# Optimization experiments

Measured on AMD Instinct MI355X. Metric: run time of the kernel, lower is better.

Reference implementation:

```python
import jax, jax.numpy as jnp
import numpy as np

DIM = 256
STATE = 64
D_INNER = 256  # ssd_expand=1 * dim
HIDDEN = 1024  # mlp_ratio=4 * dim
EPS = 1e-5


def ln2d(x, w, b):
    # channel LayerNorm over dim 1 of [B,C,H,W]
    u = x.mean(1, keepdims=True)
    s = ((x - u) ** 2).mean(1, keepdims=True)
    return w[None, :, None, None] * ((x - u) * jax.lax.rsqrt(s + EPS)) + b[None, :, None, None]


def dwconv3x3(x, w, b=None):
    # depthwise 3x3, pad 1; x [B,C,H,W], w [C,1,3,3]
    y = jax.lax.conv_general_dilated(
        x, w, (1, 1), [(1, 1), (1, 1)],
        dimension_numbers=("NCHW", "OIHW", "NCHW"),
        feature_group_count=x.shape[1])
    if b is not None:
        y = y + b[None, :, None, None]
    return y


def setup_inputs() -> dict:
    key = jax.random.key(0)
    ks = jax.random.split(key, 20)
    rn = lambda k, shp, s=0.05: (s * jax.random.normal(k, shp)).astype(jnp.float32)
    inp = {
        "x": jax.random.normal(ks[0], (16, DIM, 64, 64), dtype=jnp.float32),
        "alpha": rn(ks[1], (4, DIM), 0.1),
        "ln_w": jnp.ones((DIM,)), "ln_b": jnp.zeros((DIM,)),
        "dw1_w": rn(ks[2], (DIM, 1, 3, 3), 0.1),
        "dw1_ln_w": jnp.ones((DIM,)), "dw1_ln_b": jnp.zeros((DIM,)),
        "dw2_w": rn(ks[3], (DIM, 1, 3, 3), 0.1),
        "dw2_ln_w": jnp.ones((DIM,)), "dw2_ln_b": jnp.zeros((DIM,)),
        "bcdt_w": rn(ks[4], (3 * STATE, DIM)),
        "bcdt_b": jnp.zeros((3 * STATE,)),
        "dwm_w": rn(ks[5], (3 * STATE, 1, 3, 3), 0.1),
        "dwm_b": jnp.zeros((3 * STATE,)),
        "hz_w": rn(ks[6], (2 * D_INNER, DIM)),
        "hz_b": jnp.zeros((2 * D_INNER,)),
        "outp_w": rn(ks[7], (DIM, D_INNER)),
        "outp_b": jnp.zeros((DIM,)),
        "A": jax.random.uniform(ks[8], (STATE,), minval=1.0, maxval=16.0).astype(jnp.float32),
        "Dp": jnp.ones((DIM,)),
        "fc1_w": rn(ks[9], (HIDDEN, DIM)),
        "fc1_ln_w": jnp.ones((HIDDEN,)), "fc1_ln_b": jnp.zeros((HIDDEN,)),
        "fc2_w": rn(ks[10], (DIM, HIDDEN)),
        "fc2_ln_w": jnp.ones((DIM,)), "fc2_ln_b": jnp.zeros((DIM,)),
    }
    return inp


def reference(x, alpha, ln_w, ln_b, dw1_w, dw1_ln_w, dw1_ln_b, dw2_w, dw2_ln_w, dw2_ln_b,
              bcdt_w, bcdt_b, dwm_w, dwm_b, hz_w, hz_b, outp_w, outp_b, A, Dp,
              fc1_w, fc1_ln_w, fc1_ln_b, fc2_w, fc2_ln_w, fc2_ln_b):
    a = jax.nn.sigmoid(alpha)[:, None, :, None, None]  # [4,1,dim,1,1]

    # sub-layer 1: depthwise conv + LN, gated residual
    x1 = (1.0 - a[0]) * x + a[0] * ln2d(dwconv3x3(x, dw1_w), dw1_ln_w, dw1_ln_b)

    # HSMSSD mixer on LayerNorm2D(x1)
    xn = ln2d(x1, ln_w, ln_b)
    Bb, Dd, H, W = xn.shape
    L = H * W
    xf = xn.reshape(Bb, Dd, L)
    bcdt = jnp.einsum("oc,bcl->bol", bcdt_w, xf) + bcdt_b[None, :, None]
    bcdt = dwconv3x3(bcdt.reshape(Bb, 3 * STATE, H, W), dwm_w, dwm_b).reshape(Bb, 3 * STATE, L)
    Bm, Cm, dt = jnp.split(bcdt, [STATE, 2 * STATE], axis=1)  # each [B,S,L]
    Asm = jax.nn.softmax(dt + A[None, :, None], axis=-1)
    AB = Asm * Bm
    h = jnp.einsum("bdl,bsl->bds", xf, AB)  # [B,D,S]
    hz = jnp.einsum("oc,bcs->bos", hz_w, h) + hz_b[None, :, None]
    hp, z = jnp.split(hz, [D_INNER], axis=1)
    hg = hp * jax.nn.silu(z)
    ho = jnp.einsum("oc,bcs->bos", outp_w, hg) + outp_b[None, :, None]
    y = jnp.einsum("bds,bsl->bdl", ho, Cm).reshape(Bb, Dd, H, W)
    y = y + xn * Dp[None, :, None, None]

    x2 = (1.0 - a[1]) * x1 + a[1] * y
    x3 = (1.0 - a[2]) * x2 + a[2] * ln2d(dwconv3x3(x2, dw2_w), dw2_ln_w, dw2_ln_b)

    # FFN: 1x1 conv -> LN -> SiLU -> 1x1 conv -> LN
    f1 = jax.nn.silu(ln2d(jnp.einsum("oc,bchw->bohw", fc1_w, x3), fc1_ln_w, fc1_ln_b))
    f2 = ln2d(jnp.einsum("oc,bchw->bohw", fc2_w, f1), fc2_ln_w, fc2_ln_b)
    x4 = (1.0 - a[3]) * x3 + a[3] * f2
    return (x4, h)
```

## Files before the change

### kernel.cpp

```cpp
#include <hip/hip_runtime.h>
#include <math.h>

#define LPOS 4096
#define NB 16

typedef __bf16 bf16;
typedef __bf16 bf16x8 __attribute__((ext_vector_type(8)));
typedef __bf16 bf16x4 __attribute__((ext_vector_type(4)));
typedef float f32x4 __attribute__((ext_vector_type(4)));

#define GLOAD_LDS16(g, l) \
    __builtin_amdgcn_global_load_lds((const __attribute__((address_space(1))) unsigned int*)(g), \
                                     (__attribute__((address_space(3))) unsigned int*)(l), 16, 0, 0)

#define SWZ512(byte) ((byte) ^ (((((unsigned)(byte)) >> 9) & 7) << 4))

__device__ __forceinline__ float sigm(float x){ return 1.f/(1.f+expf(-x)); }

__global__ void dwconv3x3_k(const float* __restrict__ in, const float* __restrict__ w9,
                            const float* __restrict__ bias, float* __restrict__ out, int C)
{
    int bc = blockIdx.x;
    int c = bc % C;
    __shared__ float tile[66][72];
    const float* p = in + (size_t)bc * LPOS;
    int tid = threadIdx.x;
    for (int i = tid; i < 144; i += 256) {
        int r = (i < 72) ? 0 : 65;
        int cc = i % 72;
        tile[r][cc] = 0.f;
    }
    if (tid < 64) { tile[tid+1][3] = 0.f; tile[tid+1][68] = 0.f; }
#pragma unroll
    for (int j = 0; j < 4; j++) {
        int f = tid + j*256;
        int y = f >> 4, x4 = (f & 15) << 2;
        *(f32x4*)&tile[1+y][4+x4] = *(const f32x4*)&p[y*64 + x4];
    }
    __syncthreads();
    float w[9];
#pragma unroll
    for (int i = 0; i < 9; i++) w[i] = w9[c*9 + i];
    float bb = bias ? bias[c] : 0.f;
    float* q = out + (size_t)bc * LPOS;
#pragma unroll
    for (int j = 0; j < 4; j++) {
        int f = tid + j*256;
        int y = f >> 4, x4 = (f & 15) << 2;
        f32x4 acc = {bb, bb, bb, bb};
#pragma unroll
        for (int dy = 0; dy < 3; dy++) {
            const float* row = &tile[y+dy][3 + x4];
            float t0 = row[0], t1 = row[1], t2 = row[2];
            float t3 = row[3], t4 = row[4], t5 = row[5];
            float w0 = w[dy*3], w1 = w[dy*3+1], w2 = w[dy*3+2];
            acc[0] += w0*t0 + w1*t1 + w2*t2;
            acc[1] += w0*t1 + w1*t2 + w2*t3;
            acc[2] += w0*t2 + w1*t3 + w2*t4;
            acc[3] += w0*t3 + w1*t4 + w2*t5;
        }
        *(f32x4*)&q[y*64 + x4] = acc;
    }
}

__global__ __launch_bounds__(512)
void ln_x1xn_k(const float* __restrict__ conv, const float* __restrict__ xin,
               float* __restrict__ x1, bf16* __restrict__ xnC, bf16* __restrict__ xnT,
               const float* __restrict__ dww, const float* __restrict__ dwb,
               const float* __restrict__ g0,
               const float* __restrict__ lnw, const float* __restrict__ lnb)
{
    int b = blockIdx.x >> 6;
    int tx = threadIdx.x;
    int ty = threadIdx.y;
    int p0 = ((blockIdx.x & 63) << 6) + (tx << 2);
    __shared__ float rs[32][68], rs2[32][68];
    int tid = ty*16 + tx;
    f32x4 vals[8];
    f32x4 s = {0.f,0.f,0.f,0.f}, s2 = {0.f,0.f,0.f,0.f};
    size_t bi = ((size_t)b*256 + ty*8)*LPOS + p0;
#pragma unroll
    for (int i = 0; i < 8; i++) {
        f32x4 x = *(const f32x4*)&conv[bi + (size_t)i*LPOS];
        vals[i] = x; s += x; s2 += x*x;
    }
#pragma unroll
    for (int q = 0; q < 4; q++) { rs[ty][tx*4+q] = s[q]; rs2[ty][tx*4+q] = s2[q]; }
    __syncthreads();
    {
        int r = tid >> 6, cc = tid & 63;
        rs[r][cc]  = rs[r][cc]  + rs[r+8][cc]  + rs[r+16][cc]  + rs[r+24][cc];
        rs2[r][cc] = rs2[r][cc] + rs2[r+8][cc] + rs2[r+16][cc] + rs2[r+24][cc];
    }
    __syncthreads();
    f32x4 S = {0.f,0.f,0.f,0.f}, S2 = {0.f,0.f,0.f,0.f};
#pragma unroll
    for (int j = 0; j < 8; j++) {
        S  += *(const f32x4*)&rs[j][tx*4];
        S2 += *(const f32x4*)&rs2[j][tx*4];
    }
    f32x4 u, inv;
#pragma unroll
    for (int q = 0; q < 4; q++) {
        float uu = S[q]*(1.f/256.f);
        u[q] = uu;
        inv[q] = rsqrtf(S2[q]*(1.f/256.f) - uu*uu + 1e-5f);
    }
    __syncthreads();
    s = (f32x4){0.f,0.f,0.f,0.f}; s2 = (f32x4){0.f,0.f,0.f,0.f};
#pragma unroll
    for (int i = 0; i < 8; i++) {
        int c = ty*8 + i;
        float w = dww[c], bbc = dwb[c];
        float g = sigm(g0[c]);
        f32x4 xv = *(const f32x4*)&xin[bi + (size_t)i*LPOS];
        f32x4 r;
#pragma unroll
        for (int q = 0; q < 4; q++) {
            float ln = w*((vals[i][q]-u[q])*inv[q]) + bbc;
            r[q] = (1.f-g)*xv[q] + g*ln;
        }
        vals[i] = r;
        *(f32x4*)&x1[bi + (size_t)i*LPOS] = r;
        s += r; s2 += r*r;
    }
#pragma unroll
    for (int q = 0; q < 4; q++) { rs[ty][tx*4+q] = s[q]; rs2[ty][tx*4+q] = s2[q]; }
    __syncthreads();
    {
        int r = tid >> 6, cc = tid & 63;
        rs[r][cc]  = rs[r][cc]  + rs[r+8][cc]  + rs[r+16][cc]  + rs[r+24][cc];
        rs2[r][cc] = rs2[r][cc] + rs2[r+8][cc] + rs2[r+16][cc] + rs2[r+24][cc];
    }
    __syncthreads();
    S = (f32x4){0.f,0.f,0.f,0.f}; S2 = (f32x4){0.f,0.f,0.f,0.f};
#pragma unroll
    for (int j = 0; j < 8; j++) {
        S  += *(const f32x4*)&rs[j][tx*4];
        S2 += *(const f32x4*)&rs2[j][tx*4];
    }
#pragma unroll
    for (int q = 0; q < 4; q++) {
        float uu = S[q]*(1.f/256.f);
        u[q] = uu;
        inv[q] = rsqrtf(S2[q]*(1.f/256.f) - uu*uu + 1e-5f);
    }
    bf16 tmp[32];
#pragma unroll
    for (int i = 0; i < 8; i++) {
        int c = ty*8 + i;
        float w = lnw[c], bbc = lnb[c];
        bf16x4 o;
#pragma unroll
        for (int q = 0; q < 4; q++) {
            float xnv = w*((vals[i][q]-u[q])*inv[q]) + bbc;
            o[q] = (bf16)xnv;
            tmp[q*8+i] = (bf16)xnv;
        }
        *(bf16x4*)&xnC[bi + (size_t)i*LPOS] = o;
    }
#pragma unroll
    for (int q = 0; q < 4; q++) {
        bf16x8* dst = (bf16x8*)&xnT[((size_t)b*LPOS + p0 + q)*256 + ty*8];
        *dst = *(bf16x8*)&tmp[q*8];
    }
}

__global__ __launch_bounds__(512)
void ln2d_k(const float* __restrict__ v, const float* __restrict__ base,
            float* __restrict__ out, const float* __restrict__ lnw,
            const float* __restrict__ lnb, const float* __restrict__ gate,
            bf16* __restrict__ auxT, int mode)
{
    int b = blockIdx.x >> 6;
    int tx = threadIdx.x;
    int ty = threadIdx.y;
    int p0 = ((blockIdx.x & 63) << 6) + (tx << 2);
    __shared__ float rs[32][68], rs2[32][68];
    int tid = ty*16 + tx;
    f32x4 vals[8];
    f32x4 s = {0.f,0.f,0.f,0.f}, s2 = {0.f,0.f,0.f,0.f};
    size_t bi = ((size_t)b*256 + ty*8)*LPOS + p0;
#pragma unroll
    for (int i = 0; i < 8; i++) {
        f32x4 x = *(const f32x4*)&v[bi + (size_t)i*LPOS];
        vals[i] = x; s += x; s2 += x*x;
    }
#pragma unroll
    for (int q = 0; q < 4; q++) { rs[ty][tx*4+q] = s[q]; rs2[ty][tx*4+q] = s2[q]; }
    __syncthreads();
    {
        int r = tid >> 6, cc = tid & 63;
        rs[r][cc]  = rs[r][cc]  + rs[r+8][cc]  + rs[r+16][cc]  + rs[r+24][cc];
        rs2[r][cc] = rs2[r][cc] + rs2[r+8][cc] + rs2[r+16][cc] + rs2[r+24][cc];
    }
    __syncthreads();
    f32x4 S = {0.f,0.f,0.f,0.f}, S2 = {0.f,0.f,0.f,0.f};
#pragma unroll
    for (int j = 0; j < 8; j++) {
        S  += *(const f32x4*)&rs[j][tx*4];
        S2 += *(const f32x4*)&rs2[j][tx*4];
    }
    f32x4 u, inv;
#pragma unroll
    for (int q = 0; q < 4; q++) {
        float uu = S[q]*(1.f/256.f);
        u[q] = uu;
        inv[q] = rsqrtf(S2[q]*(1.f/256.f) - uu*uu + 1e-5f);
    }
    bf16 tmp[32];
#pragma unroll
    for (int i = 0; i < 8; i++) {
        int c = ty*8 + i;
        float w = lnw[c], bbc = lnb[c];
        f32x4 r;
        if (mode == 0) {
#pragma unroll
            for (int q = 0; q < 4; q++) r[q] = w*((vals[i][q]-u[q])*inv[q]) + bbc;
        } else {
            float g = sigm(gate[c]);
            f32x4 bs = *(const f32x4*)&base[bi + (size_t)i*LPOS];
#pragma unroll
            for (int q = 0; q < 4; q++) {
                float ln = w*((vals[i][q]-u[q])*inv[q]) + bbc;
                r[q] = (1.f-g)*bs[q] + g*ln;
            }
        }
        *(f32x4*)&out[bi + (size_t)i*LPOS] = r;
#pragma unroll
        for (int q = 0; q < 4; q++) tmp[q*8+i] = (bf16)r[q];
    }
    if (auxT) {
#pragma unroll
        for (int q = 0; q < 4; q++) {
            bf16x8* dst = (bf16x8*)&auxT[((size_t)b*LPOS + p0 + q)*256 + ty*8];
            *dst = *(bf16x8*)&tmp[q*8];
        }
    }
}

__global__ void f2b_k(const float* __restrict__ in, bf16* __restrict__ out, int n)
{
    int i = blockIdx.x*256 + threadIdx.x;
    if (i < n) out[i] = (bf16)in[i];
}

__global__ void pad_w_k(const float* __restrict__ w, bf16* __restrict__ out)
{
    int i = blockIdx.x*256 + threadIdx.x;
    int r = i >> 8;
    out[i] = (r < 192) ? (bf16)w[(size_t)r*256 + (i & 255)] : (bf16)0.f;
}

__global__ void transpose_cm_k(const float* __restrict__ Cm, bf16* __restrict__ CmT)
{
    int b = blockIdx.y;
    int l0 = blockIdx.x * 64;
    const float* src = Cm + (size_t)b * 192 * LPOS;
    bf16* dst = CmT + (size_t)b * LPOS * 64;
    __shared__ float t[64][65];
    int tid = threadIdx.x;
    for (int i = tid; i < 4096; i += 256) {
        int s = i >> 6, l = i & 63;
        t[s][l] = src[(size_t)s*LPOS + l0 + l];
    }
    __syncthreads();
    for (int i = tid; i < 4096; i += 256) {
        int l = i >> 6, s = i & 63;
        dst[(size_t)(l0+l)*64 + s] = (bf16)t[s][l];
    }
}

__global__ void softmax_ab_k(const float* __restrict__ bcdt2, bf16* __restrict__ ABb,
                             const float* __restrict__ Avec)
{
    int b = blockIdx.x >> 6, s = blockIdx.x & 63;
    size_t base = (size_t)b*192*LPOS;
    const f32x4* dt = (const f32x4*)(bcdt2 + base + (size_t)(128+s)*LPOS);
    const f32x4* Bm = (const f32x4*)(bcdt2 + base + (size_t)s*LPOS);
    bf16* outp = ABb + ((size_t)b*64 + s)*LPOS;
    int tid = threadIdx.x;
    float av = Avec[s];
    f32x4 v[4];
    float mx = -1e30f;
#pragma unroll
    for (int i = 0; i < 4; i++) {
        f32x4 x = dt[tid + (i<<8)];
#pragma unroll
        for (int q = 0; q < 4; q++) { x[q] += av; mx = fmaxf(mx, x[q]); }
        v[i] = x;
    }
    __shared__ float red[256];
    red[tid] = mx; __syncthreads();
    for (int o = 128; o > 0; o >>= 1) {
        if (tid < o) red[tid] = fmaxf(red[tid], red[tid+o]);
        __syncthreads();
    }
    mx = red[0];
    __syncthreads();
    float sum = 0.f;
#pragma unroll
    for (int i = 0; i < 4; i++)
#pragma unroll
        for (int q = 0; q < 4; q++) { v[i][q] = expf(v[i][q]-mx); sum += v[i][q]; }
    red[tid] = sum; __syncthreads();
    for (int o = 128; o > 0; o >>= 1) {
        if (tid < o) red[tid] += red[tid+o];
        __syncthreads();
    }
    float rinv = 1.f / red[0];
#pragma unroll
    for (int i = 0; i < 4; i++) {
        f32x4 bm = Bm[tid + (i<<8)];
        bf16x4 o;
#pragma unroll
        for (int q = 0; q < 4; q++) o[q] = (bf16)(v[i][q] * rinv * bm[q]);
        ((bf16x4*)outp)[tid + (i<<8)] = o;
    }
}

__global__ __launch_bounds__(512)
void mixer_tail_k(const float* __restrict__ h, const float* __restrict__ hz_w,
                  const float* __restrict__ hz_b, const float* __restrict__ outp_w,
                  const float* __restrict__ outp_b, bf16* __restrict__ hob16)
{
    __shared__ bf16 hT[64*256];
    __shared__ bf16 hzs[512*64];
    int b = blockIdx.x;
    int tid = threadIdx.x;
    int lane = tid & 63, w = tid >> 6;
    int fm = lane & 15, quad = lane >> 4;

    const float* hb = h + (size_t)b*256*64;
#pragma unroll
    for (int j = 0; j < 8; j++) {
        int e4 = tid + j*512;
        f32x4 v = *(const f32x4*)&hb[e4*4];
        int k = (e4*4) >> 6;
        int n = (e4*4) & 63;
#pragma unroll
        for (int q = 0; q < 4; q++) {
            int byte = (n+q)*512 + k*2;
            *(bf16*)((char*)hT + SWZ512(byte)) = (bf16)v[q];
        }
    }
    __syncthreads();

    int mw = w*64;
    f32x4 acc[4][4] = {};
#pragma unroll
    for (int ks = 0; ks < 8; ks++) {
        int k0 = ks*32;
        bf16x8 af[4], bfr[4];
#pragma unroll
        for (int i = 0; i < 4; i++) {
            const float* wp = &hz_w[(size_t)(mw + i*16 + fm)*256 + k0 + quad*8];
            f32x4 w0 = *(const f32x4*)wp;
            f32x4 w1 = *(const f32x4*)(wp + 4);
#pragma unroll
            for (int q = 0; q < 4; q++) { af[i][q] = (bf16)w0[q]; af[i][4+q] = (bf16)w1[q]; }
        }
#pragma unroll
        for (int j = 0; j < 4; j++) {
            int n = j*16 + fm;
            int byte = n*512 + (k0 + quad*8)*2;
            bfr[j] = *(const bf16x8*)((const char*)hT + SWZ512(byte));
        }
#pragma unroll
        for (int i = 0; i < 4; i++)
#pragma unroll
            for (int j = 0; j < 4; j++)
                acc[i][j] = __builtin_amdgcn_mfma_f32_16x16x32_bf16(af[i], bfr[j], acc[i][j], 0, 0, 0);
    }
#pragma unroll
    for (int i = 0; i < 4; i++)
#pragma unroll
        for (int r = 0; r < 4; r++) {
            int m = mw + i*16 + quad*4 + r;
            float bb = hz_b[m];
#pragma unroll
            for (int j = 0; j < 4; j++)
                hzs[m*64 + j*16 + fm] = (bf16)(acc[i][j][r] + bb);
        }
    __syncthreads();

    {
        int k = tid >> 1, n0 = (tid & 1) * 32;
#pragma unroll
        for (int c = 0; c < 4; c++) {
            bf16x8 hp = *(const bf16x8*)&hzs[k*64 + n0 + c*8];
            bf16x8 zz = *(const bf16x8*)&hzs[(k+256)*64 + n0 + c*8];
#pragma unroll
            for (int q = 0; q < 8; q++) {
                float z = (float)zz[q];
                float g = (float)hp[q] * z * sigm(z);
                int byte = (n0 + c*8 + q)*512 + k*2;
                *(bf16*)((char*)hT + SWZ512(byte)) = (bf16)g;
            }
        }
    }
    __syncthreads();

    int mw2 = w*32;
    f32x4 acc2[2][4] = {};
#pragma unroll
    for (int ks = 0; ks < 8; ks++) {
        int k0 = ks*32;
        bf16x8 af[2], bfr[4];
#pragma unroll
        for (int i = 0; i < 2; i++) {
            const float* wp = &outp_w[(size_t)(mw2 + i*16 + fm)*256 + k0 + quad*8];
            f32x4 w0 = *(const f32x4*)wp;
            f32x4 w1 = *(const f32x4*)(wp + 4);
#pragma unroll
            for (int q = 0; q < 4; q++) { af[i][q] = (bf16)w0[q]; af[i][4+q] = (bf16)w1[q]; }
        }
#pragma unroll
        for (int j = 0; j < 4; j++) {
            int n = j*16 + fm;
            int byte = n*512 + (k0 + quad*8)*2;
            bfr[j] = *(const bf16x8*)((const char*)hT + SWZ512(byte));
        }
#pragma unroll
        for (int i = 0; i < 2; i++)
#pragma unroll
            for (int j = 0; j < 4; j++)
                acc2[i][j] = __builtin_amdgcn_mfma_f32_16x16x32_bf16(af[i], bfr[j], acc2[i][j], 0, 0, 0);
    }
    bf16* ob = hob16 + (size_t)b*256*64;
#pragma unroll
    for (int i = 0; i < 2; i++)
#pragma unroll
        for (int r = 0; r < 4; r++) {
            int m = mw2 + i*16 + quad*4 + r;
            float bb = outp_b[m];
#pragma unroll
            for (int j = 0; j < 4; j++)
                ob[m*64 + j*16 + fm] = (bf16)(acc2[i][j][r] + bb);
        }
}

template<int OUT_BF16>
__global__ __launch_bounds__(256)
void gemm_nt_mfma(const bf16* __restrict__ A, const bf16* __restrict__ B,
                  void* __restrict__ C, const float* __restrict__ bias, int mlimit,
                  int K, int lda, int ldb, int ldc,
                  size_t abst, size_t bbst, size_t cbst)
{
    int b = blockIdx.z;
    const bf16* Ab = A + (size_t)b*abst;
    const bf16* Bb = B + (size_t)b*bbst;
    int m0 = blockIdx.y*128, n0 = blockIdx.x*128;
    __shared__ bf16 Asl[128*64];
    __shared__ bf16 Bsl[128*64];
    int tid = threadIdx.x;
    int lane = tid & 63;
    int w = tid >> 6;
    int wm = (w >> 1)*64, wn = (w & 1)*64;
    int fm = lane & 15, quad = lane >> 4;
    f32x4 acc[4][4] = {};
    for (int k0 = 0; k0 < K; k0 += 64) {
#pragma unroll
        for (int ii = 0; ii < 4; ii++) {
            int q = ii*256 + tid;
            int row = q >> 3, ko = (q & 7) << 3;
            GLOAD_LDS16(Ab + (size_t)(m0+row)*lda + k0 + ko, &Asl[q*8]);
            GLOAD_LDS16(Bb + (size_t)(n0+row)*ldb + k0 + ko, &Bsl[q*8]);
        }
        __syncthreads();
#pragma unroll
        for (int kk = 0; kk < 2; kk++) {
            bf16x8 af[4], bfr[4];
#pragma unroll
            for (int i = 0; i < 4; i++)
                af[i] = *(const bf16x8*)&Asl[(wm + i*16 + fm)*64 + kk*32 + quad*8];
#pragma unroll
            for (int j = 0; j < 4; j++)
                bfr[j] = *(const bf16x8*)&Bsl[(wn + j*16 + fm)*64 + kk*32 + quad*8];
#pragma unroll
            for (int i = 0; i < 4; i++)
#pragma unroll
                for (int j = 0; j < 4; j++)
                    acc[i][j] = __builtin_amdgcn_mfma_f32_16x16x32_bf16(af[i], bfr[j], acc[i][j], 0, 0, 0);
        }
        __syncthreads();
    }
    size_t cb = (size_t)b*cbst;
#pragma unroll
    for (int i = 0; i < 4; i++) {
#pragma unroll
        for (int r = 0; r < 4; r++) {
            int m = m0 + wm + i*16 + quad*4 + r;
            if (m >= mlimit) continue;
            float bb = bias ? bias[m] : 0.f;
#pragma unroll
            for (int j = 0; j < 4; j++) {
                int n = n0 + wn + j*16 + fm;
                float vv = acc[i][j][r] + bb;
                if (OUT_BF16) ((bf16*)C)[cb + (size_t)m*ldc + n] = (bf16)vv;
                else          ((float*)C)[cb + (size_t)m*ldc + n] = vv;
            }
        }
    }
}

__global__ __launch_bounds__(256)
void gemm_fc1_stats(const bf16* __restrict__ A, const bf16* __restrict__ B,
                    bf16* __restrict__ C, float* __restrict__ stats)
{
    int z = blockIdx.z;
    const bf16* Ab = A + (size_t)z*LPOS*256;
    bf16* Cb = C + (size_t)z*LPOS*1024;
    int m0 = blockIdx.y*128, n0 = blockIdx.x*128;
    __shared__ bf16 Asl[128*64];
    __shared__ bf16 Bsl[128*64];
    int tid = threadIdx.x;
    int lane = tid & 63;
    int w = tid >> 6;
    int wm = (w >> 1)*64, wn = (w & 1)*64;
    int fm = lane & 15, quad = lane >> 4;
    f32x4 acc[4][4] = {};
    for (int k0 = 0; k0 < 256; k0 += 64) {
#pragma unroll
        for (int ii = 0; ii < 4; ii++) {
            int q = ii*256 + tid;
            int row = q >> 3, ko = (q & 7) << 3;
            GLOAD_LDS16(Ab + (size_t)(m0+row)*256 + k0 + ko, &Asl[q*8]);
            GLOAD_LDS16(B + (size_t)(n0+row)*256 + k0 + ko, &Bsl[q*8]);
        }
        __syncthreads();
#pragma unroll
        for (int kk = 0; kk < 2; kk++) {
            bf16x8 af[4], bfr[4];
#pragma unroll
            for (int i = 0; i < 4; i++)
                af[i] = *(const bf16x8*)&Asl[(wm + i*16 + fm)*64 + kk*32 + quad*8];
#pragma unroll
            for (int j = 0; j < 4; j++)
                bfr[j] = *(const bf16x8*)&Bsl[(wn + j*16 + fm)*64 + kk*32 + quad*8];
#pragma unroll
            for (int i = 0; i < 4; i++)
#pragma unroll
                for (int j = 0; j < 4; j++)
                    acc[i][j] = __builtin_amdgcn_mfma_f32_16x16x32_bf16(af[i], bfr[j], acc[i][j], 0, 0, 0);
        }
        __syncthreads();
    }
#pragma unroll
    for (int i = 0; i < 4; i++) {
#pragma unroll
        for (int r = 0; r < 4; r++) {
            int m = m0 + wm + i*16 + quad*4 + r;
            float s = 0.f, s2 = 0.f;
#pragma unroll
            for (int j = 0; j < 4; j++) {
                int n = n0 + wn + j*16 + fm;
                float vv = acc[i][j][r];
                Cb[(size_t)m*1024 + n] = (bf16)vv;
                s += vv; s2 += vv*vv;
            }
#pragma unroll
            for (int msk = 1; msk <= 8; msk <<= 1) {
                s  += __shfl_xor(s, msk);
                s2 += __shfl_xor(s2, msk);
            }
            if (fm == 0) {
                atomicAdd(&stats[(size_t)(z*LPOS + m)*2 + 0], s);
                atomicAdd(&stats[(size_t)(z*LPOS + m)*2 + 1], s2);
            }
        }
    }
}

__global__ __launch_bounds__(512)
void gemm_fc2_out(const bf16* __restrict__ A, const bf16* __restrict__ f1,
                  const float* __restrict__ stats,
                  const float* __restrict__ l1w, const float* __restrict__ l1b,
                  const float* __restrict__ x3, float* __restrict__ outp,
                  const float* __restrict__ lw, const float* __restrict__ lb,
                  const float* __restrict__ gate)
{
    int z = blockIdx.z;
    const bf16* Bb = f1 + (size_t)z*LPOS*1024;
    const float* x3b = x3 + (size_t)z*256*LPOS;
    float* ob = outp + (size_t)z*256*LPOS;
    int n0 = blockIdx.x*64;
    __shared__ bf16 Asl[256*64];
    __shared__ bf16 Bsl[64*64];
    __shared__ float ps[4][64], ps2[4][64];
    __shared__ float wsl[1024], bsl[1024];
    int tid = threadIdx.x;
    int lane = tid & 63;
    int w = tid >> 6;
    int wm = (w & 3)*64, wn = (w >> 2)*32;
    int fm = lane & 15, quad = lane >> 4;
    for (int i = tid; i < 1024; i += 512) { wsl[i] = l1w[i]; bsl[i] = l1b[i]; }
    int brow = tid >> 3;
    int bko = (tid & 7) << 3;
    float sS = stats[(size_t)(z*LPOS + n0 + brow)*2 + 0];
    float sQ = stats[(size_t)(z*LPOS + n0 + brow)*2 + 1];
    float bu = sS*(1.f/1024.f);
    float binv = rsqrtf(sQ*(1.f/1024.f) - bu*bu + 1e-5f);
    f32x4 acc[4][2] = {};
    for (int k0 = 0; k0 < 1024; k0 += 64) {
#pragma unroll
        for (int ii = 0; ii < 4; ii++) {
            int q = ii*512 + tid;
            int row = q >> 3, ko = (q & 7) << 3;
            GLOAD_LDS16(A + (size_t)row*1024 + k0 + ko, &Asl[q*8]);
        }
        GLOAD_LDS16(Bb + (size_t)(n0+brow)*1024 + k0 + bko, &Bsl[tid*8]);
        __syncthreads();
        {
            bf16x8 v = *(const bf16x8*)&Bsl[tid*8];
            bf16x8 o;
#pragma unroll
            for (int e = 0; e < 8; e++) {
                int k = k0 + bko + e;
                float xx = ((float)v[e] - bu)*binv;
                xx = wsl[k]*xx + bsl[k];
                o[e] = (bf16)(xx*sigm(xx));
            }
            *(bf16x8*)&Bsl[tid*8] = o;
        }
        __syncthreads();
#pragma unroll
        for (int kk = 0; kk < 2; kk++) {
            bf16x8 af[4], bfr[2];
#pragma unroll
            for (int i = 0; i < 4; i++)
                af[i] = *(const bf16x8*)&Asl[(wm + i*16 + fm)*64 + kk*32 + quad*8];
#pragma unroll
            for (int j = 0; j < 2; j++)
                bfr[j] = *(const bf16x8*)&Bsl[(wn + j*16 + fm)*64 + kk*32 + quad*8];
#pragma unroll
            for (int i = 0; i < 4; i++)
#pragma unroll
                for (int j = 0; j < 2; j++)
                    acc[i][j] = __builtin_amdgcn_mfma_f32_16x16x32_bf16(af[i], bfr[j], acc[i][j], 0, 0, 0);
        }
        __syncthreads();
    }
#pragma unroll
    for (int j = 0; j < 2; j++) {
        float s = 0.f, s2 = 0.f;
#pragma unroll
        for (int i = 0; i < 4; i++)
#pragma unroll
            for (int r = 0; r < 4; r++) { float v = acc[i][j][r]; s += v; s2 += v*v; }
        s  += __shfl_xor(s, 16);  s2 += __shfl_xor(s2, 16);
        s  += __shfl_xor(s, 32);  s2 += __shfl_xor(s2, 32);
        if (quad == 0) {
            int n = wn + j*16 + fm;
            ps[w & 3][n] = s;
            ps2[w & 3][n] = s2;
        }
    }
    __syncthreads();
    float us[2], iv[2];
#pragma unroll
    for (int j = 0; j < 2; j++) {
        int n = wn + j*16 + fm;
        float S  = ps[0][n] + ps[1][n] + ps[2][n] + ps[3][n];
        float S2 = ps2[0][n] + ps2[1][n] + ps2[2][n] + ps2[3][n];
        float u = S*(1.f/256.f);
        us[j] = u;
        iv[j] = rsqrtf(S2*(1.f/256.f) - u*u + 1e-5f);
    }
#pragma unroll
    for (int i = 0; i < 4; i++) {
#pragma unroll
        for (int r = 0; r < 4; r++) {
            int m = wm + i*16 + quad*4 + r;
            float g = sigm(gate[m]);
            float lwm = lw[m], lbm = lb[m];
#pragma unroll
            for (int j = 0; j < 2; j++) {
                int n = n0 + wn + j*16 + fm;
                size_t idx = (size_t)m*LPOS + n;
                float ln = lwm*((acc[i][j][r]-us[j])*iv[j]) + lbm;
                ob[idx] = (1.f-g)*x3b[idx] + g*ln;
            }
        }
    }
}

__global__ __launch_bounds__(256)
void gemm_h_mfma(const bf16* __restrict__ xnC, const bf16* __restrict__ ABb,
                 float* __restrict__ h, int Kchunk)
{
    int b = blockIdx.z;
    const bf16* Ab = xnC + (size_t)b*256*LPOS;
    const bf16* Bb = ABb + (size_t)b*64*LPOS;
    float* Cb = h + (size_t)b*256*64;
    int m0 = blockIdx.y*128;
    int kbase = blockIdx.x*Kchunk;
    __shared__ bf16 Asl[128*64];
    __shared__ bf16 Bsl[64*64];
    int tid = threadIdx.x;
    int lane = tid & 63;
    int w = tid >> 6;
    int wm = (w >> 1)*64, wn = (w & 1)*32;
    int fm = lane & 15, quad = lane >> 4;
    f32x4 acc[4][2] = {};
    for (int k0 = kbase; k0 < kbase + Kchunk; k0 += 64) {
#pragma unroll
        for (int ii = 0; ii < 4; ii++) {
            int q = ii*256 + tid;
            int row = q >> 3, ko = (q & 7) << 3;
            GLOAD_LDS16(Ab + (size_t)(m0+row)*LPOS + k0 + ko, &Asl[q*8]);
        }
#pragma unroll
        for (int ii = 0; ii < 2; ii++) {
            int q = ii*256 + tid;
            int row = q >> 3, ko = (q & 7) << 3;
            GLOAD_LDS16(Bb + (size_t)row*LPOS + k0 + ko, &Bsl[q*8]);
        }
        __syncthreads();
#pragma unroll
        for (int kk = 0; kk < 2; kk++) {
            bf16x8 af[4], bfr[2];
#pragma unroll
            for (int i = 0; i < 4; i++)
                af[i] = *(const bf16x8*)&Asl[(wm + i*16 + fm)*64 + kk*32 + quad*8];
#pragma unroll
            for (int j = 0; j < 2; j++)
                bfr[j] = *(const bf16x8*)&Bsl[(wn + j*16 + fm)*64 + kk*32 + quad*8];
#pragma unroll
            for (int i = 0; i < 4; i++)
#pragma unroll
                for (int j = 0; j < 2; j++)
                    acc[i][j] = __builtin_amdgcn_mfma_f32_16x16x32_bf16(af[i], bfr[j], acc[i][j], 0, 0, 0);
        }
        __syncthreads();
    }
#pragma unroll
    for (int i = 0; i < 4; i++)
#pragma unroll
        for (int r = 0; r < 4; r++) {
            int m = m0 + wm + i*16 + quad*4 + r;
#pragma unroll
            for (int j = 0; j < 2; j++) {
                int n = wn + j*16 + fm;
                atomicAdd(&Cb[(size_t)m*64 + n], acc[i][j][r]);
            }
        }
}

__global__ __launch_bounds__(256)
void mixer_out_mfma(const bf16* __restrict__ hoB, const bf16* __restrict__ CmT,
                    const bf16* __restrict__ xnC, float* __restrict__ x,
                    const float* __restrict__ Dp, const float* __restrict__ gate)
{
    int b = blockIdx.z;
    const bf16* Ab = hoB + (size_t)b*(256*64);
    const bf16* Bb = CmT + (size_t)b*((size_t)LPOS*64);
    int m0 = blockIdx.y*128, n0 = blockIdx.x*128;
    __shared__ bf16 Asl[128*64];
    __shared__ bf16 Bsl[128*64];
    int tid = threadIdx.x;
    int lane = tid & 63;
    int w = tid >> 6;
    int wm = (w >> 1)*64, wn = (w & 1)*64;
    int fm = lane & 15, quad = lane >> 4;
    f32x4 acc[4][4] = {};
#pragma unroll
    for (int ii = 0; ii < 4; ii++) {
        int q = ii*256 + tid;
        int row = q >> 3, ko = (q & 7) << 3;
        GLOAD_LDS16(Ab + (size_t)(m0+row)*64 + ko, &Asl[q*8]);
        GLOAD_LDS16(Bb + (size_t)(n0+row)*64 + ko, &Bsl[q*8]);
    }
    __syncthreads();
#pragma unroll
    for (int kk = 0; kk < 2; kk++) {
        bf16x8 af[4], bfr[4];
#pragma unroll
        for (int i = 0; i < 4; i++)
            af[i] = *(const bf16x8*)&Asl[(wm + i*16 + fm)*64 + kk*32 + quad*8];
#pragma unroll
        for (int j = 0; j < 4; j++)
            bfr[j] = *(const bf16x8*)&Bsl[(wn + j*16 + fm)*64 + kk*32 + quad*8];
#pragma unroll
        for (int i = 0; i < 4; i++)
#pragma unroll
            for (int j = 0; j < 4; j++)
                acc[i][j] = __builtin_amdgcn_mfma_f32_16x16x32_bf16(af[i], bfr[j], acc[i][j], 0, 0, 0);
    }
#pragma unroll
    for (int i = 0; i < 4; i++) {
#pragma unroll
        for (int r = 0; r < 4; r++) {
            int m = m0 + wm + i*16 + quad*4 + r;
            float g = sigm(gate[m]);
            float dp = Dp[m];
#pragma unroll
            for (int j = 0; j < 4; j++) {
                int n = n0 + wn + j*16 + fm;
                size_t idx = ((size_t)b*256 + m)*LPOS + n;
                float y = acc[i][j][r] + (float)xnC[idx]*dp;
                x[idx] = (1.f-g)*x[idx] + g*y;
            }
        }
    }
}

extern "C" void kernel_launch(void* const* d_in, const int* in_sizes, int n_in,
                              void* d_out, int out_size, void* d_ws, size_t ws_size,
                              hipStream_t stream)
{
    const float* x        = (const float*)d_in[0];
    const float* alpha    = (const float*)d_in[1];
    const float* ln_w     = (const float*)d_in[2];
    const float* ln_b     = (const float*)d_in[3];
    const float* dw1_w    = (const float*)d_in[4];
    const float* dw1_ln_w = (const float*)d_in[5];
    const float* dw1_ln_b = (const float*)d_in[6];
    const float* dw2_w    = (const float*)d_in[7];
    const float* dw2_ln_w = (const float*)d_in[8];
    const float* dw2_ln_b = (const float*)d_in[9];
    const float* bcdt_w   = (const float*)d_in[10];
    const float* bcdt_b   = (const float*)d_in[11];
    const float* dwm_w    = (const float*)d_in[12];
    const float* dwm_b    = (const float*)d_in[13];
    const float* hz_w     = (const float*)d_in[14];
    const float* hz_b     = (const float*)d_in[15];
    const float* outp_w   = (const float*)d_in[16];
    const float* outp_b   = (const float*)d_in[17];
    const float* Avec     = (const float*)d_in[18];
    const float* Dp       = (const float*)d_in[19];
    const float* fc1_w    = (const float*)d_in[20];
    const float* fc1_ln_w = (const float*)d_in[21];
    const float* fc1_ln_b = (const float*)d_in[22];
    const float* fc2_w    = (const float*)d_in[23];
    const float* fc2_ln_w = (const float*)d_in[24];
    const float* fc2_ln_b = (const float*)d_in[25];

    float* outp  = (float*)d_out;
    float* h_out = outp + (size_t)NB*256*LPOS;

    float* ws   = (float*)d_ws;
    float* bufA = ws;
    float* bufB = bufA + (size_t)NB*256*LPOS;
    float* bufC = bufB + (size_t)NB*256*LPOS;
    float* bufD = bufC + (size_t)NB*256*LPOS;
    float* hzb  = bufD + (size_t)NB*192*LPOS;

    bf16* CmT     = (bf16*)bufA;
    bf16* ABb     = (bf16*)(bufA + 8*1024*1024);
    bf16* xnC     = (bf16*)bufC;
    bf16* xnT     = xnC + (size_t)NB*256*LPOS;
    bf16* f1buf   = (bf16*)bufC;
    bf16* x3t     = (bf16*)bufD;
    bf16* fc1_wb  = (bf16*)(bufD + 9000000);
    bf16* fc2_wb  = (bf16*)(bufD + 9200000);
    bf16* hob16   = (bf16*)(bufD + 9400000);
    float* stats  = bufD + 10000000;
    bf16* wpad    = (bf16*)hzb;

    dim3 blk256(256);
    dim3 blkLN(16, 32);

    dwconv3x3_k<<<dim3(NB*256), blk256, 0, stream>>>(x, dw1_w, nullptr, bufA, 256);
    ln_x1xn_k<<<dim3(NB*64), blkLN, 0, stream>>>(bufA, x, bufB, xnC, xnT,
                                                 dw1_ln_w, dw1_ln_b, alpha + 0, ln_w, ln_b);
    pad_w_k<<<dim3(256), blk256, 0, stream>>>(bcdt_w, wpad);
    gemm_nt_mfma<0><<<dim3(32, 2, NB), blk256, 0, stream>>>(
        wpad, xnT, (void*)bufA, bcdt_b, 192, 256, 256, 256, LPOS,
        0, (size_t)LPOS*256, (size_t)192*LPOS);
    dwconv3x3_k<<<dim3(NB*192), blk256, 0, stream>>>(bufA, dwm_w, dwm_b, bufD, 192);
    transpose_cm_k<<<dim3(64, NB), blk256, 0, stream>>>(bufD + (size_t)64*LPOS, CmT);
    softmax_ab_k<<<dim3(NB*64), blk256, 0, stream>>>(bufD, ABb, Avec);
    hipMemsetAsync(h_out, 0, (size_t)NB*256*64*sizeof(float), stream);
    gemm_h_mfma<<<dim3(4, 2, NB), blk256, 0, stream>>>(xnC, ABb, h_out, 1024);
    mixer_tail_k<<<dim3(NB), dim3(512), 0, stream>>>(h_out, hz_w, hz_b, outp_w, outp_b, hob16);
    f2b_k<<<dim3(1024), blk256, 0, stream>>>(fc1_w, fc1_wb, 1024*256);
    f2b_k<<<dim3(1024), blk256, 0, stream>>>(fc2_w, fc2_wb, 256*1024);
    mixer_out_mfma<<<dim3(32, 2, NB), blk256, 0, stream>>>(hob16, CmT, xnC, bufB, Dp, alpha + 256);
    dwconv3x3_k<<<dim3(NB*256), blk256, 0, stream>>>(bufB, dw2_w, nullptr, bufA, 256);
    ln2d_k<<<dim3(NB*64), blkLN, 0, stream>>>(bufA, bufB, bufB, dw2_ln_w, dw2_ln_b, alpha + 512, x3t, 1);
    for (int ch = 0; ch < 4; ch++) {
        const bf16*  x3tc = x3t + (size_t)ch*4*LPOS*256;
        const float* x3c  = bufB + (size_t)ch*4*256*LPOS;
        float* outc = outp + (size_t)ch*4*256*LPOS;
        hipMemsetAsync(stats, 0, (size_t)4*LPOS*2*sizeof(float), stream);
        gemm_fc1_stats<<<dim3(8, 32, 4), blk256, 0, stream>>>(x3tc, fc1_wb, f1buf, stats);
        gemm_fc2_out<<<dim3(64, 1, 4), dim3(512), 0, stream>>>(
            fc2_wb, f1buf, stats, fc1_ln_w, fc1_ln_b, x3c, outc, fc2_ln_w, fc2_ln_b, alpha + 768);
    }
}
```

Before: 756.0 us.

## XOR-swizzle fc2 LDS tiles and batch FFN chunks of eight into two buffers

The fc2 GEMM now XOR-swizzles the 16-byte chunk index by row when loading A and B tiles into LDS and when reading fragments, to avoid LDS bank conflicts on the MFMA fragment reads. The FFN loop now processes 8 batch images per chunk instead of 4, writing fc1 output into two separate buffers (bufA and bufC). A single fc2 launch covers all 8 images with a doubled grid. This halves the number of fc2 launches and memsets and gives each fc2 launch more blocks, at the cost of reusing bufA as scratch, which must no longer be live.

```diff
diff --git a/kernel.cpp b/kernel.cpp
--- a/kernel.cpp
+++ b/kernel.cpp
@@ -573,15 +573,15 @@
 }
 
 __global__ __launch_bounds__(512)
-void gemm_fc2_out(const bf16* __restrict__ A, const bf16* __restrict__ f1,
-                  const float* __restrict__ stats,
+void gemm_fc2_out(const bf16* __restrict__ A, const bf16* __restrict__ f1a,
+                  const bf16* __restrict__ f1b, const float* __restrict__ stats,
                   const float* __restrict__ l1w, const float* __restrict__ l1b,
                   const float* __restrict__ x3, float* __restrict__ outp,
                   const float* __restrict__ lw, const float* __restrict__ lb,
                   const float* __restrict__ gate)
 {
     int z = blockIdx.z;
-    const bf16* Bb = f1 + (size_t)z*LPOS*1024;
+    const bf16* Bb = (z < 4 ? f1a + (size_t)z*LPOS*1024 : f1b + (size_t)(z-4)*LPOS*1024);
     const float* x3b = x3 + (size_t)z*256*LPOS;
     float* ob = outp + (size_t)z*256*LPOS;
     int n0 = blockIdx.x*64;
@@ -596,7 +596,7 @@
     int fm = lane & 15, quad = lane >> 4;
     for (int i = tid; i < 1024; i += 512) { wsl[i] = l1w[i]; bsl[i] = l1b[i]; }
     int brow = tid >> 3;
-    int bko = (tid & 7) << 3;
+    int bko = (((tid & 7) ^ (brow & 7))) << 3;
     float sS = stats[(size_t)(z*LPOS + n0 + brow)*2 + 0];
     float sQ = stats[(size_t)(z*LPOS + n0 + brow)*2 + 1];
     float bu = sS*(1.f/1024.f);
@@ -606,7 +606,7 @@
 #pragma unroll
         for (int ii = 0; ii < 4; ii++) {
             int q = ii*512 + tid;
-            int row = q >> 3, ko = (q & 7) << 3;
+            int row = q >> 3, ko = (((q & 7) ^ (row & 7))) << 3;
             GLOAD_LDS16(A + (size_t)row*1024 + k0 + ko, &Asl[q*8]);
         }
         GLOAD_LDS16(Bb + (size_t)(n0+brow)*1024 + k0 + bko, &Bsl[tid*8]);
@@ -628,11 +628,15 @@
         for (int kk = 0; kk < 2; kk++) {
             bf16x8 af[4], bfr[2];
 #pragma unroll
-            for (int i = 0; i < 4; i++)
-                af[i] = *(const bf16x8*)&Asl[(wm + i*16 + fm)*64 + kk*32 + quad*8];
-#pragma unroll
-            for (int j = 0; j < 2; j++)
-                bfr[j] = *(const bf16x8*)&Bsl[(wn + j*16 + fm)*64 + kk*32 + quad*8];
+            for (int i = 0; i < 4; i++) {
+                int R = wm + i*16 + fm;
+                af[i] = *(const bf16x8*)&Asl[R*64 + (((kk*4 + quad) ^ (R & 7)))*8];
+            }
+#pragma unroll
+            for (int j = 0; j < 2; j++) {
+                int R = wn + j*16 + fm;
+                bfr[j] = *(const bf16x8*)&Bsl[R*64 + (((kk*4 + quad) ^ (R & 7)))*8];
+            }
 #pragma unroll
             for (int i = 0; i < 4; i++)
 #pragma unroll
@@ -850,7 +854,8 @@
     bf16* ABb     = (bf16*)(bufA + 8*1024*1024);
     bf16* xnC     = (bf16*)bufC;
     bf16* xnT     = xnC + (size_t)NB*256*LPOS;
-    bf16* f1buf   = (bf16*)bufC;
+    bf16* f1a     = (bf16*)bufA;
+    bf16* f1b     = (bf16*)bufC;
     bf16* x3t     = (bf16*)bufD;
     bf16* fc1_wb  = (bf16*)(bufD + 9000000);
     bf16* fc2_wb  = (bf16*)(bufD + 9200000);
@@ -879,13 +884,17 @@
     mixer_out_mfma<<<dim3(32, 2, NB), blk256, 0, stream>>>(hob16, CmT, xnC, bufB, Dp, alpha + 256);
     dwconv3x3_k<<<dim3(NB*256), blk256, 0, stream>>>(bufB, dw2_w, nullptr, bufA, 256);
     ln2d_k<<<dim3(NB*64), blkLN, 0, stream>>>(bufA, bufB, bufB, dw2_ln_w, dw2_ln_b, alpha + 512, x3t, 1);
-    for (int ch = 0; ch < 4; ch++) {
-        const bf16*  x3tc = x3t + (size_t)ch*4*LPOS*256;
-        const float* x3c  = bufB + (size_t)ch*4*256*LPOS;
-        float* outc = outp + (size_t)ch*4*256*LPOS;
-        hipMemsetAsync(stats, 0, (size_t)4*LPOS*2*sizeof(float), stream);
-        gemm_fc1_stats<<<dim3(8, 32, 4), blk256, 0, stream>>>(x3tc, fc1_wb, f1buf, stats);
-        gemm_fc2_out<<<dim3(64, 1, 4), dim3(512), 0, stream>>>(
-            fc2_wb, f1buf, stats, fc1_ln_w, fc1_ln_b, x3c, outc, fc2_ln_w, fc2_ln_b, alpha + 768);
-    }
-}
+    for (int ch = 0; ch < 2; ch++) {
+        const bf16*  x3tA = x3t + (size_t)(ch*8 + 0)*LPOS*256;
+        const bf16*  x3tB = x3t + (size_t)(ch*8 + 4)*LPOS*256;
+        const float* x3c  = bufB + (size_t)ch*8*256*LPOS;
+        float* outc = outp + (size_t)ch*8*256*LPOS;
+        hipMemsetAsync(stats, 0, (size_t)8*LPOS*2*sizeof(float), stream);
+        gemm_fc1_stats<<<dim3(8, 32, 4), blk256, 0, stream>>>(x3tA, fc1_wb, f1a, stats);
+        gemm_fc1_stats<<<dim3(8, 32, 4), blk256, 0, stream>>>(x3tB, fc1_wb, f1b,
+                                                              stats + (size_t)4*LPOS*2);
+        gemm_fc2_out<<<dim3(64, 1, 8), dim3(512), 0, stream>>>(
+            fc2_wb, f1a, f1b, stats, fc1_ln_w, fc1_ln_b, x3c, outc,
+            fc2_ln_w, fc2_ln_b, alpha + 768);
+    }
+}
```

New measurement: 681.7 us. 1.11x faster.
